# Performance work log

Measured on AMD Instinct MI355X. Metric: run time of the kernel, lower is better.

## Reference

```python
import jax, jax.numpy as jnp
import numpy as np

SS = 25.0 / 255.0   # spatial_scale = 1 / (SEARCH_SIZE/25), SEARCH_SIZE = 255
OUT = 7             # ROIPOOL_OUTSIZE // 4, ROIPOOL_OUTSIZE = 28
SP = 4              # sample_per_part (mmdet DeformRoIPooling default)
TRANS_STD = 0.1


def _deform_roi_pool(x, rois, offset):
    # x: [B,C,H,W]; rois: [N,5] (batch_idx,x1,y1,x2,y2); offset: [N,2,OUT,OUT] (ch0=x, ch1=y)
    B, C, H, W = x.shape
    N = rois.shape[0]
    b = rois[:, 0].astype(jnp.int32)
    sw = jnp.round(rois[:, 1]) * SS - 0.5
    sh = jnp.round(rois[:, 2]) * SS - 0.5
    rw = jnp.maximum((jnp.round(rois[:, 3]) + 1.0) * SS - 0.5 - sw, 0.1)
    rh = jnp.maximum((jnp.round(rois[:, 4]) + 1.0) * SS - 0.5 - sh, 0.1)
    bw, bh = rw / OUT, rh / OUT
    p = jnp.arange(OUT, dtype=x.dtype)
    tx = offset[:, 0] * TRANS_STD  # [N,OUT,OUT] indexed [n,ph,pw]
    ty = offset[:, 1] * TRANS_STD
    wstart = p[None, None, :] * bw[:, None, None] + sw[:, None, None] + tx * rw[:, None, None]
    hstart = p[None, :, None] * bh[:, None, None] + sh[:, None, None] + ty * rh[:, None, None]
    s = jnp.arange(SP, dtype=x.dtype)
    # sample coords [N,OUT,OUT,SP(ih),SP(iw)]
    sx = wstart[..., None, None] + s[None, None, None, None, :] * (bw / SP)[:, None, None, None, None]
    sy = hstart[..., None, None] + s[None, None, None, :, None] * (bh / SP)[:, None, None, None, None]
    valid = (sx >= -0.5) & (sx <= W - 0.5) & (sy >= -0.5) & (sy <= H - 0.5)
    xc = jnp.clip(sx, 0.0, W - 1.0)
    yc = jnp.clip(sy, 0.0, H - 1.0)
    x0 = jnp.floor(xc)
    y0 = jnp.floor(yc)
    dx = xc - x0
    dy = yc - y0
    xi0 = x0.astype(jnp.int32)
    yi0 = y0.astype(jnp.int32)
    xi1 = jnp.ceil(xc).astype(jnp.int32)
    yi1 = jnp.ceil(yc).astype(jnp.int32)
    feat = jnp.transpose(x, (0, 2, 3, 1))  # [B,H,W,C]
    bb = b[:, None, None, None, None]

    def g(yi, xi):
        return feat[bb, yi, xi]  # [N,OUT,OUT,SP,SP,C]

    val = (((1 - dx) * (1 - dy))[..., None] * g(yi0, xi0)
           + (dx * (1 - dy))[..., None] * g(yi0, xi1)
           + ((1 - dx) * dy)[..., None] * g(yi1, xi0)
           + (dx * dy)[..., None] * g(yi1, xi1))
    val = jnp.where(valid[..., None], val, 0.0)
    cnt = valid.sum(axis=(3, 4)).astype(x.dtype)              # [N,OUT,OUT]
    pooled = val.sum(axis=(3, 4)) / jnp.maximum(cnt, 1.0)[..., None]
    return jnp.transpose(pooled, (0, 3, 1, 2))                # [N,C,OUT,OUT]


def _lin(h, w, b):
    return h @ w.T + b


def _forward(x, rois, off_w1, off_b1, off_w2, off_b2, off_w3, off_b3,
             fc1_w, fc1_b, fc2_w, fc2_b, box_w, box_b):
    N = rois.shape[0]
    zero_off = jnp.zeros((N, 2, OUT, OUT), x.dtype)
    # pass 1: no-trans pooling -> offset prediction
    p0 = _deform_roi_pool(x, rois, zero_off).reshape(N, -1)
    h = jax.nn.relu(_lin(p0, off_w1, off_b1))
    h = jax.nn.relu(_lin(h, off_w2, off_b2))
    off = _lin(h, off_w3, off_b3).reshape(N, 2, OUT, OUT)
    # pass 2: deformable pooling with predicted offsets
    p = _deform_roi_pool(x, rois, off).reshape(N, -1)
    h = jax.nn.relu(_lin(p, fc1_w, fc1_b))
    h = jax.nn.relu(_lin(h, fc2_w, fc2_b))
    return _lin(h, box_w, box_b)  # [N,4]


def setup_inputs():
    key = jax.random.key(0)
    ks = jax.random.split(key, 16)
    B, C, H, W, N = 8, 256, 25, 25, 256
    IN = C * OUT * OUT  # 12544
    DFC, FCC = 1024, 512
    x = jax.random.normal(ks[0], (B, C, H, W), jnp.float32)
    bidx = jax.random.randint(ks[1], (N,), 0, B).astype(jnp.float32)
    x1 = jax.random.uniform(ks[2], (N,), minval=0.0, maxval=180.0)
    y1 = jax.random.uniform(ks[3], (N,), minval=0.0, maxval=180.0)
    wd = jax.random.uniform(ks[4], (N,), minval=24.0, maxval=120.0)
    ht = jax.random.uniform(ks[5], (N,), minval=24.0, maxval=120.0)
    rois = jnp.stack([bidx, x1, y1, jnp.clip(x1 + wd, 0.0, 254.0),
                      jnp.clip(y1 + ht, 0.0, 254.0)], axis=1)

    def lin_p(k, o, i):
        return jax.random.normal(k, (o, i), jnp.float32) * (1.0 / np.sqrt(i))

    return dict(
        x=x, rois=rois,
        off_w1=lin_p(ks[6], DFC, IN), off_b1=jnp.zeros((DFC,), jnp.float32),
        off_w2=lin_p(ks[7], DFC, DFC), off_b2=jnp.zeros((DFC,), jnp.float32),
        off_w3=lin_p(ks[8], 2 * OUT * OUT, DFC) * 0.1,
        off_b3=jnp.zeros((2 * OUT * OUT,), jnp.float32),
        fc1_w=lin_p(ks[9], FCC, IN), fc1_b=jnp.zeros((FCC,), jnp.float32),
        fc2_w=lin_p(ks[10], FCC, FCC), fc2_b=jnp.zeros((FCC,), jnp.float32),
        box_w=lin_p(ks[11], 4, FCC) * 0.001, box_b=jnp.zeros((4,), jnp.float32),
    )


def reference(x, rois, off_w1, off_b1, off_w2, off_b2, off_w3, off_b3,
              fc1_w, fc1_b, fc2_w, fc2_b, box_w, box_b):
    return _forward(x, rois, off_w1, off_b1, off_w2, off_b2, off_w3, off_b3,
                    fc1_w, fc1_b, fc2_w, fc2_b, box_w, box_b)
```

## Files before the change

### kernel.cpp

```cpp
#include <hip/hip_runtime.h>
#include <hip/hip_bf16.h>


#define NROI 256
#define NB   8
#define INF  12544
#define DFC  1024
#define FCC  512

typedef __attribute__((ext_vector_type(8))) short short8;
typedef __attribute__((ext_vector_type(4))) float floatx4;

static __device__ __forceinline__ unsigned short f2bf(float f) {
    unsigned int u = __float_as_uint(f);
    unsigned int r = (u + 0x7fffu + ((u >> 16) & 1u)) >> 16;
    return (unsigned short)r;
}

static __device__ __forceinline__ void async_copy16(const void* g, void* l) {
    __builtin_amdgcn_global_load_lds(
        (const __attribute__((address_space(1))) unsigned int*)g,
        (__attribute__((address_space(3))) unsigned int*)l, 16, 0, 0);
}

__global__ __launch_bounds__(256) void transpose_kernel(
        const float* __restrict__ x, float* __restrict__ xT) {
    __shared__ float t[32][33];
    int b  = blockIdx.z;
    int cb = blockIdx.y * 32;
    int lb = blockIdx.x * 32;
    int tx = threadIdx.x & 31, ty = threadIdx.x >> 5;
#pragma unroll
    for (int r = 0; r < 4; ++r) {
        int c = cb + ty + r * 8, l = lb + tx;
        if (l < 625) t[ty + r * 8][tx] = x[(size_t)(b * 256 + c) * 625 + l];
    }
    __syncthreads();
#pragma unroll
    for (int r = 0; r < 4; ++r) {
        int l = lb + ty + r * 8, c = cb + tx;
        if (l < 625) xT[((size_t)b * 625 + l) * 256 + c] = t[tx][ty + r * 8];
    }
}

__global__ __launch_bounds__(256) void pool_prep(
        const float* __restrict__ rois, const float* __restrict__ off, int has_off,
        float* __restrict__ wbuf, int* __restrict__ bbuf) {
    __shared__ float g[256][16];
    const float SSC = (float)(25.0 / 255.0);
    int tid = threadIdx.x;
    int idx = blockIdx.x * 256 + tid;
    int n = idx / 49;
    int bin = idx - n * 49;
    const float* r = rois + n * 5;
    int b = (int)r[0];
    float sw = rintf(r[1]) * SSC - 0.5f;
    float sh = rintf(r[2]) * SSC - 0.5f;
    float rw = fmaxf((rintf(r[3]) + 1.0f) * SSC - 0.5f - sw, 0.1f);
    float rh = fmaxf((rintf(r[4]) + 1.0f) * SSC - 0.5f - sh, 0.1f);
    float bw = rw / 7.0f, bh = rh / 7.0f;
    float bws = bw * 0.25f, bhs = bh * 0.25f;
    int ph = bin / 7, pw = bin - ph * 7;
    float tx = 0.f, ty = 0.f;
    if (has_off) {
        tx = off[n * 98 + bin] * 0.1f;
        ty = off[n * 98 + 49 + bin] * 0.1f;
    }
    float wstart = pw * bw + sw + tx * rw;
    float hstart = ph * bh + sh + ty * rh;
#pragma unroll
    for (int i = 0; i < 16; ++i) g[tid][i] = 0.f;
    int gy0 = 0, gx0 = 0, cnt = 0;
#pragma unroll
    for (int s = 0; s < 16; ++s) {
        float fx = wstart + (s & 3) * bws;
        float fy = hstart + (s >> 2) * bhs;
        bool valid = (fx >= -0.5f) && (fx <= 24.5f) && (fy >= -0.5f) && (fy <= 24.5f);
        float xc = fminf(fmaxf(fx, 0.f), 24.f);
        float yc = fminf(fmaxf(fy, 0.f), 24.f);
        float x0f = floorf(xc), y0f = floorf(yc);
        float dx = xc - x0f, dy = yc - y0f;
        int x0 = (int)x0f, y0 = (int)y0f;
        int x1 = (int)ceilf(xc), y1 = (int)ceilf(yc);
        if (s == 0) { gy0 = y0; gx0 = x0; }
        float w00 = (1.f - dx) * (1.f - dy), w01 = dx * (1.f - dy);
        float w10 = (1.f - dx) * dy,         w11 = dx * dy;
        if (!valid) { w00 = w01 = w10 = w11 = 0.f; }
        cnt += valid ? 1 : 0;
        int ry0 = (y0 - gy0) * 4, ry1 = (y1 - gy0) * 4;
        g[tid][ry0 + (x0 - gx0)] += w00;
        g[tid][ry0 + (x1 - gx0)] += w01;
        g[tid][ry1 + (x0 - gx0)] += w10;
        g[tid][ry1 + (x1 - gx0)] += w11;
    }
    float inv = 1.0f / fmaxf((float)cnt, 1.0f);
    float4* wp = (float4*)(wbuf + (size_t)idx * 16);
#pragma unroll
    for (int q = 0; q < 4; ++q)
        wp[q] = make_float4(g[tid][q * 4] * inv, g[tid][q * 4 + 1] * inv,
                            g[tid][q * 4 + 2] * inv, g[tid][q * 4 + 3] * inv);
    bbuf[idx] = gy0 | (gx0 << 8) | (b << 16);
}

__global__ __launch_bounds__(256) void pool_gather(
        const float* __restrict__ feat, const float* __restrict__ wbuf,
        const int* __restrict__ bbuf, unsigned short* __restrict__ P) {
    __shared__ unsigned short sOut[128 * 49];
    int q = blockIdx.x;
    int n = blockIdx.y;
    int tid = threadIdx.x;
    int wv = tid >> 6, lane = tid & 63;
    int cbase = q * 128 + lane * 2;

    for (int bin = wv; bin < 49; bin += 4) {
        int di = n * 49 + bin;
        int base = bbuf[di];
        int gy0 = base & 255, gx0 = (base >> 8) & 255, b = base >> 16;
        const float4* wp = (const float4*)(wbuf + (size_t)di * 16);
        float4 w0 = wp[0], w1 = wp[1], w2 = wp[2], w3 = wp[3];
        float ww[16] = { w0.x, w0.y, w0.z, w0.w, w1.x, w1.y, w1.z, w1.w,
                         w2.x, w2.y, w2.z, w2.w, w3.x, w3.y, w3.z, w3.w };
        int rowOff[4], colOff[4];
#pragma unroll
        for (int r = 0; r < 4; ++r) {
            rowOff[r] = min(gy0 + r, 24) * 25;
            colOff[r] = min(gx0 + r, 24);
        }
        int b625 = b * 625;
        float ax = 0.f, ay = 0.f;
#pragma unroll
        for (int cell = 0; cell < 16; ++cell) {
            int pix = b625 + rowOff[cell >> 2] + colOff[cell & 3];
            float2 v = *(const float2*)(feat + (size_t)pix * 256 + cbase);
            ax += ww[cell] * v.x;
            ay += ww[cell] * v.y;
        }
        sOut[(lane * 2) * 49 + bin] = f2bf(ax);
        sOut[(lane * 2 + 1) * 49 + bin] = f2bf(ay);
    }
    __syncthreads();
    const uint2* so = (const uint2*)sOut;
    uint2* dp = (uint2*)(P + (size_t)n * INF + q * 128 * 49);
    for (int i = tid; i < 128 * 49 / 4; i += 256) dp[i] = so[i];
}

template <int BN>
__global__ __launch_bounds__(256) void gemm_nt_part(
        const unsigned short* __restrict__ A, const float* __restrict__ Bw,
        float* __restrict__ Cpart, int N, int K, int kSteps) {
    constexpr int BM = 256;
    constexpr int LDB = 40;
    __shared__ unsigned short As[BM * 32];
    __shared__ unsigned short Bs[BN * LDB];
    const int tid = threadIdx.x;
    const int lane = tid & 63;
    const int wave = tid >> 6;
    const int n0 = blockIdx.x * BN;
    const int k0 = blockIdx.z * kSteps * 32;
    const int quad = lane >> 4;
    const int l16 = lane & 15;
    constexpr int FM = 4, FN = BN / 16;

    floatx4 acc[FM][FN];
#pragma unroll
    for (int i = 0; i < FM; ++i)
#pragma unroll
        for (int j = 0; j < FN; ++j) acc[i][j] = (floatx4)0.f;

    const unsigned short* agp[4];
    void* alp[4];
#pragma unroll
    for (int i = 0; i < 4; ++i) {
        int idx = tid + i * 256;
        int row = idx >> 2;
        int qq = (idx & 3) ^ ((row >> 1) & 3);
        agp[i] = A + (size_t)row * K + qq * 8;
        alp[i] = (char*)As + ((size_t)i * 256 + wave * 64) * 16;
    }
    const int brow = tid >> 3, bq = tid & 7;
    const float* bgp = Bw + (size_t)(n0 + brow) * K + bq * 4;
    unsigned short* blp = Bs + brow * LDB + bq * 4;

    float4 bv = *(const float4*)(bgp + k0);
    for (int ks = 0; ks < kSteps; ++ks) {
        int kk = k0 + ks * 32;
        __syncthreads();
#pragma unroll
        for (int i = 0; i < 4; ++i)
            async_copy16(agp[i] + kk, alp[i]);
        {
            ushort4 h;
            h.x = f2bf(bv.x); h.y = f2bf(bv.y); h.z = f2bf(bv.z); h.w = f2bf(bv.w);
            *(ushort4*)blp = h;
        }
        if (ks + 1 < kSteps) bv = *(const float4*)(bgp + kk + 32);
        __syncthreads();
        short8 a[FM], bfr[FN];
#pragma unroll
        for (int i = 0; i < FM; ++i) {
            int r = wave * 64 + i * 16 + l16;
            int slot = quad ^ ((r >> 1) & 3);
            a[i] = *(const short8*)(As + r * 32 + slot * 8);
        }
#pragma unroll
        for (int j = 0; j < FN; ++j)
            bfr[j] = *(const short8*)(Bs + (j * 16 + l16) * LDB + quad * 8);
#pragma unroll
        for (int i = 0; i < FM; ++i)
#pragma unroll
            for (int j = 0; j < FN; ++j)
                acc[i][j] = __builtin_amdgcn_mfma_f32_16x16x32_bf16(a[i], bfr[j], acc[i][j], 0, 0, 0);
    }
    float* Cp = Cpart + (size_t)blockIdx.z * BM * N;
#pragma unroll
    for (int i = 0; i < FM; ++i)
#pragma unroll
        for (int rr = 0; rr < 4; ++rr) {
            int row = wave * 64 + i * 16 + quad * 4 + rr;
            float* cr = Cp + (size_t)row * N + n0;
#pragma unroll
            for (int j = 0; j < FN; ++j)
                cr[j * 16 + l16] = acc[i][j][rr];
        }
}

__global__ __launch_bounds__(256) void reduce_bias(
        const float* __restrict__ part, int zc, int mn4,
        const float* __restrict__ bias, int nmask, int relu,
        unsigned short* __restrict__ obf, float* __restrict__ of) {
    int idx = blockIdx.x * 256 + threadIdx.x;
    if (idx >= mn4) return;
    int idx4 = idx * 4;
    const float* bp = bias + (idx4 & nmask);
    float4 acc = *(const float4*)bp;
    const float4* p = (const float4*)part + idx;
    for (int z = 0; z < zc; ++z) {
        float4 v = p[(size_t)z * mn4];
        acc.x += v.x; acc.y += v.y; acc.z += v.z; acc.w += v.w;
    }
    if (relu) {
        acc.x = fmaxf(acc.x, 0.f); acc.y = fmaxf(acc.y, 0.f);
        acc.z = fmaxf(acc.z, 0.f); acc.w = fmaxf(acc.w, 0.f);
    }
    if (obf) {
        ushort4 h;
        h.x = f2bf(acc.x); h.y = f2bf(acc.y); h.z = f2bf(acc.z); h.w = f2bf(acc.w);
        *(ushort4*)(obf + idx4) = h;
    }
    if (of) *(float4*)(of + idx4) = acc;
}

__global__ __launch_bounds__(128) void fc_small(
        const float* __restrict__ h2, const float* __restrict__ w3,
        const float* __restrict__ b3, float* __restrict__ out) {
    __shared__ float shl[1024];
    int n = blockIdx.x, tid = threadIdx.x;
    for (int i = tid; i < 1024; i += 128) shl[i] = fmaxf(h2[(size_t)n * 1024 + i], 0.f);
    __syncthreads();
    if (tid < 98) {
        float acc = b3[tid];
        const float* w = w3 + (size_t)tid * 1024;
        for (int k = 0; k < 1024; k += 4) {
            float4 wv = *(const float4*)(w + k);
            acc += shl[k] * wv.x + shl[k + 1] * wv.y + shl[k + 2] * wv.z + shl[k + 3] * wv.w;
        }
        out[n * 98 + tid] = acc;
    }
}

__global__ __launch_bounds__(64) void head_kernel(
        const float* __restrict__ h4, const float* __restrict__ bw,
        const float* __restrict__ bb, float* __restrict__ out) {
    int n = blockIdx.x, t = threadIdx.x;
    float a0 = 0, a1 = 0, a2 = 0, a3 = 0;
    for (int k = t; k < 512; k += 64) {
        float v = fmaxf(h4[(size_t)n * 512 + k], 0.f);
        a0 += v * bw[k]; a1 += v * bw[512 + k];
        a2 += v * bw[1024 + k]; a3 += v * bw[1536 + k];
    }
#pragma unroll
    for (int o = 32; o > 0; o >>= 1) {
        a0 += __shfl_down(a0, o); a1 += __shfl_down(a1, o);
        a2 += __shfl_down(a2, o); a3 += __shfl_down(a3, o);
    }
    if (t == 0) {
        out[n * 4 + 0] = a0 + bb[0]; out[n * 4 + 1] = a1 + bb[1];
        out[n * 4 + 2] = a2 + bb[2]; out[n * 4 + 3] = a3 + bb[3];
    }
}

extern "C" void kernel_launch(void* const* d_in, const int* in_sizes, int n_in,
                              void* d_out, int out_size, void* d_ws, size_t ws_size,
                              hipStream_t stream) {
    const float* x      = (const float*)d_in[0];
    const float* rois   = (const float*)d_in[1];
    const float* off_w1 = (const float*)d_in[2];
    const float* off_b1 = (const float*)d_in[3];
    const float* off_w2 = (const float*)d_in[4];
    const float* off_b2 = (const float*)d_in[5];
    const float* off_w3 = (const float*)d_in[6];
    const float* off_b3 = (const float*)d_in[7];
    const float* fc1_w  = (const float*)d_in[8];
    const float* fc1_b  = (const float*)d_in[9];
    const float* fc2_w  = (const float*)d_in[10];
    const float* fc2_b  = (const float*)d_in[11];
    const float* box_w  = (const float*)d_in[12];
    const float* box_b  = (const float*)d_in[13];
    float* out = (float*)d_out;

    char* ws = (char*)d_ws;
    size_t o = 0;
    auto carve = [&](size_t bytes) { char* p = ws + o; o += (bytes + 255) & ~(size_t)255; return p; };
    float*          xT   = (float*)carve((size_t)NB * 625 * 256 * 4);
    unsigned short* P    = (unsigned short*)carve((size_t)NROI * INF * 2);
    unsigned short* h1b  = (unsigned short*)carve((size_t)NROI * DFC * 2);
    float*          h2   = (float*)carve((size_t)NROI * DFC * 4);
    float*          offb = (float*)carve((size_t)NROI * 98 * 4);
    unsigned short* h3b  = (unsigned short*)carve((size_t)NROI * FCC * 2);
    float*          h4   = (float*)carve((size_t)NROI * FCC * 4);
    float*          wbuf = (float*)carve((size_t)NROI * 49 * 16 * 4);
    int*            bbuf = (int*)carve((size_t)NROI * 49 * 4);
    size_t fixed = o;
    const size_t SLAB = (size_t)NROI * DFC * 4;
    int zg1;
    if      (ws_size >= fixed + 28 * SLAB) zg1 = 28;
    else if (ws_size >= fixed + 14 * SLAB) zg1 = 14;
    else                                   zg1 = 7;
    int zg2 = (zg1 >= 8) ? 8 : 4;
    float* part = (float*)carve((size_t)zg1 * SLAB);

    transpose_kernel<<<dim3(20, 8, 8), 256, 0, stream>>>(x, xT);
    pool_prep<<<49, 256, 0, stream>>>(rois, nullptr, 0, wbuf, bbuf);
    pool_gather<<<dim3(2, NROI), 256, 0, stream>>>(xT, wbuf, bbuf, P);
    gemm_nt_part<32><<<dim3(32, 1, zg1), 256, 0, stream>>>(P, off_w1, part, DFC, INF, 392 / zg1);
    reduce_bias<<<256, 256, 0, stream>>>(part, zg1, NROI * DFC / 4, off_b1, DFC - 1, 1, h1b, nullptr);
    gemm_nt_part<32><<<dim3(32, 1, zg2), 256, 0, stream>>>(h1b, off_w2, part, DFC, DFC, 32 / zg2);
    reduce_bias<<<256, 256, 0, stream>>>(part, zg2, NROI * DFC / 4, off_b2, DFC - 1, 0, nullptr, h2);
    fc_small<<<NROI, 128, 0, stream>>>(h2, off_w3, off_b3, offb);
    pool_prep<<<49, 256, 0, stream>>>(rois, offb, 1, wbuf, bbuf);
    pool_gather<<<dim3(2, NROI), 256, 0, stream>>>(xT, wbuf, bbuf, P);
    gemm_nt_part<32><<<dim3(16, 1, zg1), 256, 0, stream>>>(P, fc1_w, part, FCC, INF, 392 / zg1);
    reduce_bias<<<128, 256, 0, stream>>>(part, zg1, NROI * FCC / 4, fc1_b, FCC - 1, 1, h3b, nullptr);
    gemm_nt_part<32><<<dim3(16, 1, zg2), 256, 0, stream>>>(h3b, fc2_w, part, FCC, FCC, 16 / zg2);
    reduce_bias<<<128, 256, 0, stream>>>(part, zg2, NROI * FCC / 4, fc2_b, FCC - 1, 0, nullptr, h4);
    head_kernel<<<NROI, 64, 0, stream>>>(h4, box_w, box_b, out);
}
```

Before: 315.5 us.

## Fuse pool prep into gather, triple-buffer async GEMM loads, batch fc_small

Merges pool_prep into the gather kernel so each block computes its bin weights in shared memory, which removes a launch and the wbuf/bbuf round trip. The GEMM becomes a 3-stage pipeline in which both A (bf16) and the fp32 weights B are loaded with async global-to-LDS copies, using an XOR swizzle on B and converting B to bf16 at fragment-load time. Waits are manual vmcnt plus barrier. fc_small now handles two ROIs per block, and the second-layer split-K factor is fixed at 8. The cost is more LDS per GEMM block, redundant weight computation across the two q blocks of each ROI, and fragile hand-written waitcnt logic.

```diff
diff --git a/kernel.cpp b/kernel.cpp
--- a/kernel.cpp
+++ b/kernel.cpp
@@ -43,80 +43,74 @@
     }
 }
 
-__global__ __launch_bounds__(256) void pool_prep(
-        const float* __restrict__ rois, const float* __restrict__ off, int has_off,
-        float* __restrict__ wbuf, int* __restrict__ bbuf) {
-    __shared__ float g[256][16];
+__global__ __launch_bounds__(256) void pool_kernel(
+        const float* __restrict__ feat, const float* __restrict__ rois,
+        const float* __restrict__ off, int has_off,
+        unsigned short* __restrict__ P) {
+    __shared__ float sGrid[49][16];
+    __shared__ int   sBase[49];
+    __shared__ unsigned short sOut[128 * 49];
     const float SSC = (float)(25.0 / 255.0);
-    int tid = threadIdx.x;
-    int idx = blockIdx.x * 256 + tid;
-    int n = idx / 49;
-    int bin = idx - n * 49;
-    const float* r = rois + n * 5;
-    int b = (int)r[0];
-    float sw = rintf(r[1]) * SSC - 0.5f;
-    float sh = rintf(r[2]) * SSC - 0.5f;
-    float rw = fmaxf((rintf(r[3]) + 1.0f) * SSC - 0.5f - sw, 0.1f);
-    float rh = fmaxf((rintf(r[4]) + 1.0f) * SSC - 0.5f - sh, 0.1f);
-    float bw = rw / 7.0f, bh = rh / 7.0f;
-    float bws = bw * 0.25f, bhs = bh * 0.25f;
-    int ph = bin / 7, pw = bin - ph * 7;
-    float tx = 0.f, ty = 0.f;
-    if (has_off) {
-        tx = off[n * 98 + bin] * 0.1f;
-        ty = off[n * 98 + 49 + bin] * 0.1f;
-    }
-    float wstart = pw * bw + sw + tx * rw;
-    float hstart = ph * bh + sh + ty * rh;
-#pragma unroll
-    for (int i = 0; i < 16; ++i) g[tid][i] = 0.f;
-    int gy0 = 0, gx0 = 0, cnt = 0;
-#pragma unroll
-    for (int s = 0; s < 16; ++s) {
-        float fx = wstart + (s & 3) * bws;
-        float fy = hstart + (s >> 2) * bhs;
-        bool valid = (fx >= -0.5f) && (fx <= 24.5f) && (fy >= -0.5f) && (fy <= 24.5f);
-        float xc = fminf(fmaxf(fx, 0.f), 24.f);
-        float yc = fminf(fmaxf(fy, 0.f), 24.f);
-        float x0f = floorf(xc), y0f = floorf(yc);
-        float dx = xc - x0f, dy = yc - y0f;
-        int x0 = (int)x0f, y0 = (int)y0f;
-        int x1 = (int)ceilf(xc), y1 = (int)ceilf(yc);
-        if (s == 0) { gy0 = y0; gx0 = x0; }
-        float w00 = (1.f - dx) * (1.f - dy), w01 = dx * (1.f - dy);
-        float w10 = (1.f - dx) * dy,         w11 = dx * dy;
-        if (!valid) { w00 = w01 = w10 = w11 = 0.f; }
-        cnt += valid ? 1 : 0;
-        int ry0 = (y0 - gy0) * 4, ry1 = (y1 - gy0) * 4;
-        g[tid][ry0 + (x0 - gx0)] += w00;
-        g[tid][ry0 + (x1 - gx0)] += w01;
-        g[tid][ry1 + (x0 - gx0)] += w10;
-        g[tid][ry1 + (x1 - gx0)] += w11;
-    }
-    float inv = 1.0f / fmaxf((float)cnt, 1.0f);
-    float4* wp = (float4*)(wbuf + (size_t)idx * 16);
-#pragma unroll
-    for (int q = 0; q < 4; ++q)
-        wp[q] = make_float4(g[tid][q * 4] * inv, g[tid][q * 4 + 1] * inv,
-                            g[tid][q * 4 + 2] * inv, g[tid][q * 4 + 3] * inv);
-    bbuf[idx] = gy0 | (gx0 << 8) | (b << 16);
-}
-
-__global__ __launch_bounds__(256) void pool_gather(
-        const float* __restrict__ feat, const float* __restrict__ wbuf,
-        const int* __restrict__ bbuf, unsigned short* __restrict__ P) {
-    __shared__ unsigned short sOut[128 * 49];
     int q = blockIdx.x;
     int n = blockIdx.y;
     int tid = threadIdx.x;
+
+    if (tid < 49) {
+        int bin = tid;
+        const float* r = rois + n * 5;
+        int b = (int)r[0];
+        float sw = rintf(r[1]) * SSC - 0.5f;
+        float sh = rintf(r[2]) * SSC - 0.5f;
+        float rw = fmaxf((rintf(r[3]) + 1.0f) * SSC - 0.5f - sw, 0.1f);
+        float rh = fmaxf((rintf(r[4]) + 1.0f) * SSC - 0.5f - sh, 0.1f);
+        float bw = rw / 7.0f, bh = rh / 7.0f;
+        float bws = bw * 0.25f, bhs = bh * 0.25f;
+        int ph = bin / 7, pw = bin - ph * 7;
+        float tx = 0.f, ty = 0.f;
+        if (has_off) {
+            tx = off[n * 98 + bin] * 0.1f;
+            ty = off[n * 98 + 49 + bin] * 0.1f;
+        }
+        float wstart = pw * bw + sw + tx * rw;
+        float hstart = ph * bh + sh + ty * rh;
+#pragma unroll
+        for (int i = 0; i < 16; ++i) sGrid[bin][i] = 0.f;
+        int gy0 = 0, gx0 = 0, cnt = 0;
+#pragma unroll
+        for (int s = 0; s < 16; ++s) {
+            float fx = wstart + (s & 3) * bws;
+            float fy = hstart + (s >> 2) * bhs;
+            bool valid = (fx >= -0.5f) && (fx <= 24.5f) && (fy >= -0.5f) && (fy <= 24.5f);
+            float xc = fminf(fmaxf(fx, 0.f), 24.f);
+            float yc = fminf(fmaxf(fy, 0.f), 24.f);
+            float x0f = floorf(xc), y0f = floorf(yc);
+            float dx = xc - x0f, dy = yc - y0f;
+            int x0 = (int)x0f, y0 = (int)y0f;
+            int x1 = (int)ceilf(xc), y1 = (int)ceilf(yc);
+            if (s == 0) { gy0 = y0; gx0 = x0; }
+            float w00 = (1.f - dx) * (1.f - dy), w01 = dx * (1.f - dy);
+            float w10 = (1.f - dx) * dy,         w11 = dx * dy;
+            if (!valid) { w00 = w01 = w10 = w11 = 0.f; }
+            cnt += valid ? 1 : 0;
+            int ry0 = (y0 - gy0) * 4, ry1 = (y1 - gy0) * 4;
+            sGrid[bin][ry0 + (x0 - gx0)] += w00;
+            sGrid[bin][ry0 + (x1 - gx0)] += w01;
+            sGrid[bin][ry1 + (x0 - gx0)] += w10;
+            sGrid[bin][ry1 + (x1 - gx0)] += w11;
+        }
+        float inv = 1.0f / fmaxf((float)cnt, 1.0f);
+#pragma unroll
+        for (int i = 0; i < 16; ++i) sGrid[bin][i] *= inv;
+        sBase[bin] = gy0 | (gx0 << 8) | (b << 16);
+    }
+    __syncthreads();
+
     int wv = tid >> 6, lane = tid & 63;
     int cbase = q * 128 + lane * 2;
-
     for (int bin = wv; bin < 49; bin += 4) {
-        int di = n * 49 + bin;
-        int base = bbuf[di];
+        int base = sBase[bin];
         int gy0 = base & 255, gx0 = (base >> 8) & 255, b = base >> 16;
-        const float4* wp = (const float4*)(wbuf + (size_t)di * 16);
+        const float4* wp = (const float4*)sGrid[bin];
         float4 w0 = wp[0], w1 = wp[1], w2 = wp[2], w3 = wp[3];
         float ww[16] = { w0.x, w0.y, w0.z, w0.w, w1.x, w1.y, w1.z, w1.w,
                          w2.x, w2.y, w2.z, w2.w, w3.x, w3.y, w3.z, w3.w };
@@ -144,14 +138,13 @@
     for (int i = tid; i < 128 * 49 / 4; i += 256) dp[i] = so[i];
 }
 
-template <int BN>
-__global__ __launch_bounds__(256) void gemm_nt_part(
+__global__ __launch_bounds__(256) void gemm_pipe(
         const unsigned short* __restrict__ A, const float* __restrict__ Bw,
         float* __restrict__ Cpart, int N, int K, int kSteps) {
-    constexpr int BM = 256;
-    constexpr int LDB = 40;
-    __shared__ unsigned short As[BM * 32];
-    __shared__ unsigned short Bs[BN * LDB];
+    constexpr int BM = 256, BN = 32, D = 3;
+    constexpr int FM = 4, FN = 2;
+    __shared__ unsigned short As[D][BM * 32];
+    __shared__ float          Bs[D][BN * 32];
     const int tid = threadIdx.x;
     const int lane = tid & 63;
     const int wave = tid >> 6;
@@ -159,7 +152,6 @@
     const int k0 = blockIdx.z * kSteps * 32;
     const int quad = lane >> 4;
     const int l16 = lane & 15;
-    constexpr int FM = 4, FN = BN / 16;
 
     floatx4 acc[FM][FN];
 #pragma unroll
@@ -167,49 +159,67 @@
 #pragma unroll
         for (int j = 0; j < FN; ++j) acc[i][j] = (floatx4)0.f;
 
-    const unsigned short* agp[4];
-    void* alp[4];
+    const unsigned short* ag[4];
+    int albase[4];
 #pragma unroll
     for (int i = 0; i < 4; ++i) {
         int idx = tid + i * 256;
         int row = idx >> 2;
-        int qq = (idx & 3) ^ ((row >> 1) & 3);
-        agp[i] = A + (size_t)row * K + qq * 8;
-        alp[i] = (char*)As + ((size_t)i * 256 + wave * 64) * 16;
-    }
-    const int brow = tid >> 3, bq = tid & 7;
-    const float* bgp = Bw + (size_t)(n0 + brow) * K + bq * 4;
-    unsigned short* blp = Bs + brow * LDB + bq * 4;
-
-    float4 bv = *(const float4*)(bgp + k0);
+        int kg4 = (idx & 3) ^ ((row >> 1) & 3);
+        ag[i] = A + (size_t)row * K + kg4 * 8;
+        albase[i] = (i * 256 + wave * 64) * 16;
+    }
+    const int brow = tid >> 3;
+    const int bkg = (tid & 7) ^ ((brow >> 1) & 7);
+    const float* bg = Bw + (size_t)(n0 + brow) * K + bkg * 4;
+    const int blbase = wave * 64 * 16;
+
+    auto issue = [&](int slot, int kk) {
+#pragma unroll
+        for (int i = 0; i < 4; ++i)
+            async_copy16(ag[i] + kk, (char*)&As[slot][0] + albase[i]);
+        async_copy16(bg + kk, (char*)&Bs[slot][0] + blbase);
+    };
+
+#pragma unroll
+    for (int p = 0; p < D - 1; ++p) {
+        int pk = (p < kSteps) ? p : (kSteps - 1);
+        issue(p, k0 + pk * 32);
+    }
+
+    int cur = 0;
     for (int ks = 0; ks < kSteps; ++ks) {
-        int kk = k0 + ks * 32;
-        __syncthreads();
-#pragma unroll
-        for (int i = 0; i < 4; ++i)
-            async_copy16(agp[i] + kk, alp[i]);
-        {
-            ushort4 h;
-            h.x = f2bf(bv.x); h.y = f2bf(bv.y); h.z = f2bf(bv.z); h.w = f2bf(bv.w);
-            *(ushort4*)blp = h;
-        }
-        if (ks + 1 < kSteps) bv = *(const float4*)(bgp + kk + 32);
-        __syncthreads();
-        short8 a[FM], bfr[FN];
+        asm volatile("s_waitcnt vmcnt(5)" ::: "memory");
+        asm volatile("s_barrier" ::: "memory");
+        int pfs = cur + D - 1; if (pfs >= D) pfs -= D;
+        int pfk = ks + D - 1; if (pfk >= kSteps) pfk = kSteps - 1;
+        issue(pfs, k0 + pfk * 32);
+        short8 a[FM], bf[FN];
 #pragma unroll
         for (int i = 0; i < FM; ++i) {
             int r = wave * 64 + i * 16 + l16;
-            int slot = quad ^ ((r >> 1) & 3);
-            a[i] = *(const short8*)(As + r * 32 + slot * 8);
-        }
-#pragma unroll
-        for (int j = 0; j < FN; ++j)
-            bfr[j] = *(const short8*)(Bs + (j * 16 + l16) * LDB + quad * 8);
+            int sl = quad ^ ((r >> 1) & 3);
+            a[i] = *(const short8*)(&As[cur][0] + r * 32 + sl * 8);
+        }
+#pragma unroll
+        for (int j = 0; j < FN; ++j) {
+            int r = j * 16 + l16;
+            int sw8 = (r >> 1) & 7;
+            int g0 = (quad * 2) ^ sw8;
+            int g1 = (quad * 2 + 1) ^ sw8;
+            float4 v0 = *(const float4*)(&Bs[cur][0] + r * 32 + g0 * 4);
+            float4 v1 = *(const float4*)(&Bs[cur][0] + r * 32 + g1 * 4);
+            bf[j][0] = (short)f2bf(v0.x); bf[j][1] = (short)f2bf(v0.y);
+            bf[j][2] = (short)f2bf(v0.z); bf[j][3] = (short)f2bf(v0.w);
+            bf[j][4] = (short)f2bf(v1.x); bf[j][5] = (short)f2bf(v1.y);
+            bf[j][6] = (short)f2bf(v1.z); bf[j][7] = (short)f2bf(v1.w);
+        }
 #pragma unroll
         for (int i = 0; i < FM; ++i)
 #pragma unroll
             for (int j = 0; j < FN; ++j)
-                acc[i][j] = __builtin_amdgcn_mfma_f32_16x16x32_bf16(a[i], bfr[j], acc[i][j], 0, 0, 0);
+                acc[i][j] = __builtin_amdgcn_mfma_f32_16x16x32_bf16(a[i], bf[j], acc[i][j], 0, 0, 0);
+        cur = cur + 1; if (cur >= D) cur = 0;
     }
     float* Cp = Cpart + (size_t)blockIdx.z * BM * N;
 #pragma unroll
@@ -250,21 +260,25 @@
     if (of) *(float4*)(of + idx4) = acc;
 }
 
-__global__ __launch_bounds__(128) void fc_small(
+__global__ __launch_bounds__(256) void fc_small(
         const float* __restrict__ h2, const float* __restrict__ w3,
         const float* __restrict__ b3, float* __restrict__ out) {
-    __shared__ float shl[1024];
-    int n = blockIdx.x, tid = threadIdx.x;
-    for (int i = tid; i < 1024; i += 128) shl[i] = fmaxf(h2[(size_t)n * 1024 + i], 0.f);
+    __shared__ float shl[2][1024];
+    int n2 = blockIdx.x * 2;
+    int tid = threadIdx.x;
+    for (int i = tid; i < 2048; i += 256)
+        shl[i >> 10][i & 1023] = fmaxf(h2[(size_t)n2 * 1024 + i], 0.f);
     __syncthreads();
-    if (tid < 98) {
-        float acc = b3[tid];
-        const float* w = w3 + (size_t)tid * 1024;
+    int h = tid >> 7, o = tid & 127;
+    if (o < 98) {
+        float acc = b3[o];
+        const float* w = w3 + (size_t)o * 1024;
+        const float* s = shl[h];
         for (int k = 0; k < 1024; k += 4) {
             float4 wv = *(const float4*)(w + k);
-            acc += shl[k] * wv.x + shl[k + 1] * wv.y + shl[k + 2] * wv.z + shl[k + 3] * wv.w;
-        }
-        out[n * 98 + tid] = acc;
+            acc += s[k] * wv.x + s[k + 1] * wv.y + s[k + 2] * wv.z + s[k + 3] * wv.w;
+        }
+        out[(n2 + h) * 98 + o] = acc;
     }
 }
 
@@ -318,30 +332,25 @@
     float*          offb = (float*)carve((size_t)NROI * 98 * 4);
     unsigned short* h3b  = (unsigned short*)carve((size_t)NROI * FCC * 2);
     float*          h4   = (float*)carve((size_t)NROI * FCC * 4);
-    float*          wbuf = (float*)carve((size_t)NROI * 49 * 16 * 4);
-    int*            bbuf = (int*)carve((size_t)NROI * 49 * 4);
     size_t fixed = o;
     const size_t SLAB = (size_t)NROI * DFC * 4;
     int zg1;
     if      (ws_size >= fixed + 28 * SLAB) zg1 = 28;
     else if (ws_size >= fixed + 14 * SLAB) zg1 = 14;
     else                                   zg1 = 7;
-    int zg2 = (zg1 >= 8) ? 8 : 4;
     float* part = (float*)carve((size_t)zg1 * SLAB);
 
     transpose_kernel<<<dim3(20, 8, 8), 256, 0, stream>>>(x, xT);
-    pool_prep<<<49, 256, 0, stream>>>(rois, nullptr, 0, wbuf, bbuf);
-    pool_gather<<<dim3(2, NROI), 256, 0, stream>>>(xT, wbuf, bbuf, P);
-    gemm_nt_part<32><<<dim3(32, 1, zg1), 256, 0, stream>>>(P, off_w1, part, DFC, INF, 392 / zg1);
+    pool_kernel<<<dim3(2, NROI), 256, 0, stream>>>(xT, rois, nullptr, 0, P);
+    gemm_pipe<<<dim3(32, 1, zg1), 256, 0, stream>>>(P, off_w1, part, DFC, INF, 392 / zg1);
     reduce_bias<<<256, 256, 0, stream>>>(part, zg1, NROI * DFC / 4, off_b1, DFC - 1, 1, h1b, nullptr);
-    gemm_nt_part<32><<<dim3(32, 1, zg2), 256, 0, stream>>>(h1b, off_w2, part, DFC, DFC, 32 / zg2);
-    reduce_bias<<<256, 256, 0, stream>>>(part, zg2, NROI * DFC / 4, off_b2, DFC - 1, 0, nullptr, h2);
-    fc_small<<<NROI, 128, 0, stream>>>(h2, off_w3, off_b3, offb);
-    pool_prep<<<49, 256, 0, stream>>>(rois, offb, 1, wbuf, bbuf);
-    pool_gather<<<dim3(2, NROI), 256, 0, stream>>>(xT, wbuf, bbuf, P);
-    gemm_nt_part<32><<<dim3(16, 1, zg1), 256, 0, stream>>>(P, fc1_w, part, FCC, INF, 392 / zg1);
+    gemm_pipe<<<dim3(32, 1, 8), 256, 0, stream>>>(h1b, off_w2, part, DFC, DFC, 4);
+    reduce_bias<<<256, 256, 0, stream>>>(part, 8, NROI * DFC / 4, off_b2, DFC - 1, 0, nullptr, h2);
+    fc_small<<<128, 256, 0, stream>>>(h2, off_w3, off_b3, offb);
+    pool_kernel<<<dim3(2, NROI), 256, 0, stream>>>(xT, rois, offb, 1, P);
+    gemm_pipe<<<dim3(16, 1, zg1), 256, 0, stream>>>(P, fc1_w, part, FCC, INF, 392 / zg1);
     reduce_bias<<<128, 256, 0, stream>>>(part, zg1, NROI * FCC / 4, fc1_b, FCC - 1, 1, h3b, nullptr);
-    gemm_nt_part<32><<<dim3(16, 1, zg2), 256, 0, stream>>>(h3b, fc2_w, part, FCC, FCC, 16 / zg2);
-    reduce_bias<<<128, 256, 0, stream>>>(part, zg2, NROI * FCC / 4, fc2_b, FCC - 1, 0, nullptr, h4);
+    gemm_pipe<<<dim3(16, 1, 8), 256, 0, stream>>>(h3b, fc2_w, part, FCC, FCC, 2);
+    reduce_bias<<<128, 256, 0, stream>>>(part, 8, NROI * FCC / 4, fc2_b, FCC - 1, 0, nullptr, h4);
     head_kernel<<<NROI, 64, 0, stream>>>(h4, box_w, box_b, out);
 }
```

Measured after the change: 302.7 us. 1.04x faster.
